# Kernel optimization log

Hardware: AMD Instinct MI355X
Metric: run time of the kernel (lower is better)

The kernel has to match this reference:

```python
import jax, jax.numpy as jnp
from jax import lax
import numpy as np

N, K, QK, W = 10, 10, 150, 128
D = 256
HID = 100
CHANS = [1, 16, 32, 64, 128, 256]
STRIDES = [2, 2, 1, 1, 1]
ITERS = 3
BN_EPS = 1e-5


def setup_inputs() -> dict:
    key = jax.random.key(0)
    ks = jax.random.split(key, 12)
    inp = {
        "support": jax.random.normal(ks[0], (N, K, 1, W, W), jnp.float32),
        "query": jax.random.normal(ks[1], (QK, 1, W, W), jnp.float32),
    }
    for i in range(5):
        inp[f"conv_w{i}"] = jax.random.normal(ks[2 + i], (CHANS[i + 1], CHANS[i], 3, 3), jnp.float32) * 0.05
        inp[f"bn_g{i}"] = jnp.ones((CHANS[i + 1],), jnp.float32)
        inp[f"bn_b{i}"] = jnp.zeros((CHANS[i + 1],), jnp.float32)
    inp["trans_w"] = jax.random.normal(ks[8], (D, D), jnp.float32) * 0.05
    inp["trans_b"] = jnp.zeros((D,), jnp.float32)
    inp["bil_w"] = jax.random.normal(ks[9], (HID, D, D), jnp.float32) * 0.02
    inp["score_w"] = jax.random.normal(ks[10], (1, HID), jnp.float32) * 0.1
    inp["score_b"] = jnp.zeros((1,), jnp.float32)
    return inp


def _block(x, w, g, b, s):
    # Conv2d(k=3, pad=1, stride=s, no bias) -> BatchNorm(eval: mean=0, var=1) -> ReLU -> MaxPool2d(2)
    x = lax.conv_general_dilated(x, w, (s, s), ((1, 1), (1, 1)),
                                 dimension_numbers=('NCHW', 'OIHW', 'NCHW'))
    scale = (g / jnp.sqrt(1.0 + BN_EPS))[None, :, None, None]
    x = jax.nn.relu(x * scale + b[None, :, None, None])
    return lax.reduce_window(x, -jnp.inf, lax.max, (1, 1, 2, 2), (1, 1, 2, 2), 'VALID')


def reference(support, query,
              conv_w0, conv_w1, conv_w2, conv_w3, conv_w4,
              bn_g0, bn_g1, bn_g2, bn_g3, bn_g4,
              bn_b0, bn_b1, bn_b2, bn_b3, bn_b4,
              trans_w, trans_b, bil_w, score_w, score_b):
    n, k = support.shape[0], support.shape[1]
    qk = query.shape[0]
    w = support.shape[3]

    ws = [conv_w0, conv_w1, conv_w2, conv_w3, conv_w4]
    gs = [bn_g0, bn_g1, bn_g2, bn_g3, bn_g4]
    bs = [bn_b0, bn_b1, bn_b2, bn_b3, bn_b4]

    # run the conv backbone on support+query jointly (BN is per-sample in eval mode)
    x = jnp.concatenate([support.reshape(n * k, 1, w, w), query], axis=0)
    for cw, g, b, s in zip(ws, gs, bs, STRIDES):
        x = _block(x, cw, g, b, s)
    feats = x.reshape(x.shape[0], -1)              # (n*k + qk, 256); spatial is 1x1
    sup = feats[:n * k].reshape(n, k, -1)          # (n, k, d)
    q = feats[n * k:]                              # (qk, d)

    # dynamic routing: Transformer(e) is recomputed each iter on the same input -> hoist
    e = sup @ trans_w.T + trans_b                  # (n, k, d)
    b0 = jnp.zeros((n, k), sup.dtype)

    def step(bb, _):
        dcoef = jax.nn.softmax(bb, axis=1)[:, :, None]   # (n, k, 1)
        c = (dcoef * e).sum(axis=1)                      # (n, d)
        cn = jnp.sqrt((c * c).sum(axis=1, keepdims=True))
        c = c * (cn / (cn * cn + 1.0))                   # squash: ||c||^2/(||c||^2+1)/||c||
        db = (c[:, None, :] * e).sum(axis=2)             # (n, k)
        return bb + db, c

    _, cs = lax.scan(step, b0, None, length=ITERS)
    proto = cs[-1]                                  # (n, d)

    # NTN: bilinear score for every (query, proto) pair, exploiting the pair structure
    t1 = jnp.einsum('nc,hce->nhe', proto, bil_w)    # (n, HID, d)
    v = jnp.einsum('nhe,qe->qnh', t1, q)            # (qk, n, HID)
    s = jax.nn.relu(v) @ score_w[0] + score_b[0]    # (qk, n)
    return jax.nn.log_softmax(s, axis=1)
```

## Files before the change

kernel.cpp:

```cpp
#include <hip/hip_runtime.h>
#include <math.h>


#define BN_SCALE rsqrtf(1.0f + 1e-5f)

#define OFF_FEATS 0
#define OFF_E     64000
#define OFF_S     89600
#define OFF_T1    91136
#define OFF_PROTO 347136
#define OFF_W1T   349696
#define OFF_W2T   354304
#define OFF_W3T   372736
#define OFF_W4T   446464
#define OFF_TWT   741376

__global__ void k_prep(const float* __restrict__ w1, const float* __restrict__ w2,
                       const float* __restrict__ w3, const float* __restrict__ w4,
                       const float* __restrict__ tw, float* __restrict__ ws) {
  float* w1t = ws + OFF_W1T;
  float* w2t = ws + OFF_W2T;
  float* w3t = ws + OFF_W3T;
  float* w4t = ws + OFF_W4T;
  float* twt = ws + OFF_TWT;
  int i = blockIdx.x * 256 + threadIdx.x;
  if (i < 4608) {
    int oc = i / 144, r = i % 144;
    int ic = r / 9, tap = r % 9;
    w1t[(ic * 9 + tap) * 32 + oc] = w1[i];
  } else if (i < 23040) {
    int m = i - 4608;
    int oc = m / 288, r = m % 288;
    int ic = r / 9, tap = r % 9;
    w2t[(ic * 9 + tap) * 64 + oc] = w2[m];
  } else if (i < 96768) {
    int m = i - 23040;
    int oc = m / 576, r = m % 576;
    int ic = r / 9, tap = r % 9;
    w3t[(ic * 9 + tap) * 128 + oc] = w3[m];
  } else if (i < 391680) {
    int m = i - 96768;
    int oc = m / 1152, r = m % 1152;
    int ic = r / 9, tap = r % 9;
    w4t[(ic * 9 + tap) * 256 + oc] = w4[m];
  } else if (i < 457216) {
    int m = i - 391680;
    int r = m >> 8, s = m & 255;
    twt[s * 256 + r] = tw[m];
  } else if (i < 713216) {
    ws[OFF_T1 + (i - 457216)] = 0.f;
  } else if (i < 714716) {
    ws[OFF_S + (i - 713216)] = 0.f;
  }
}

__global__ void __launch_bounds__(1024, 4)
k_main(const float* __restrict__ sup, const float* __restrict__ qry,
       const float* __restrict__ w0, const float* __restrict__ g0, const float* __restrict__ b0,
       const float* __restrict__ g1, const float* __restrict__ b1,
       const float* __restrict__ g2, const float* __restrict__ b2,
       const float* __restrict__ g3, const float* __restrict__ b3,
       const float* __restrict__ g4, const float* __restrict__ b4,
       const float* __restrict__ tb, float* __restrict__ ws,
       float* __restrict__ feats_g, float* __restrict__ e_buf) {
  __shared__ __align__(16) float S[38404];
  const float* w1t = ws + OFF_W1T;
  const float* w2t = ws + OFF_W2T;
  const float* w3t = ws + OFF_W3T;
  const float* w4t = ws + OFF_W4T;
  const float* twt = ws + OFF_TWT;
  const int img = blockIdx.x;
  const int t = threadIdx.x;
  const int lane = t & 63, wid = t >> 6;
  float* sa1 = S;
  float* sa2 = S + 4096;
  float* sa3 = S + 7424;
  float* sft = S + 7936;
  float* a0p = S + 8580;
  float* RED = S + 8580;
  float* L1R = S + 28164;

  const float* in = (img < 100) ? (sup + (size_t)img * 16384)
                                : (qry + (size_t)(img - 100) * 16384);

  {
    float4* S4 = (float4*)S;
    const float4 z4 = make_float4(0.f, 0.f, 0.f, 0.f);
    for (int i = t; i < 7041; i += 1024) S4[i] = z4;
  }
  __syncthreads();

  {
    const int ocp = wid & 7;
    const int rhalf = wid >> 3;
    const int oc0 = 2 * ocp, oc1 = oc0 + 1;
    float wv0[9], wv1[9];
#pragma unroll
    for (int k = 0; k < 9; k++) { wv0[k] = w0[oc0 * 9 + k]; wv1[k] = w0[oc1 * 9 + k]; }
    const float sc0 = g0[oc0] * BN_SCALE, bs0 = b0[oc0];
    const float sc1 = g0[oc1] * BN_SCALE, bs1 = b0[oc1];
#pragma unroll
    for (int it2 = 0; it2 < 2; it2++) {
      const int s2 = rhalf * 128 + it2 * 64 + lane;
      const int pr = s2 >> 3, pcq = s2 & 7;
      float ac0[2][8], ac1[2][8];
#pragma unroll
      for (int j = 0; j < 8; j++) {
        ac0[0][j] = 0.f; ac0[1][j] = 0.f; ac1[0][j] = 0.f; ac1[1][j] = 0.f;
      }
#pragma unroll
      for (int d = 0; d < 5; d++) {
        const int ir = 4 * pr - 1 + d;
        float x[17];
        if (ir >= 0) {
          const float* rp = in + ir * 128 + 16 * pcq;
          float4 q0 = ((const float4*)rp)[0];
          float4 q1 = ((const float4*)rp)[1];
          float4 q2 = ((const float4*)rp)[2];
          float4 q3 = ((const float4*)rp)[3];
          x[0] = (pcq > 0) ? rp[-1] : 0.f;
          x[1] = q0.x;  x[2] = q0.y;  x[3] = q0.z;  x[4] = q0.w;
          x[5] = q1.x;  x[6] = q1.y;  x[7] = q1.z;  x[8] = q1.w;
          x[9] = q2.x;  x[10] = q2.y; x[11] = q2.z; x[12] = q2.w;
          x[13] = q3.x; x[14] = q3.y; x[15] = q3.z; x[16] = q3.w;
        } else {
#pragma unroll
          for (int k = 0; k < 17; k++) x[k] = 0.f;
        }
        if (d <= 2) {
          const int b9 = d * 3;
#pragma unroll
          for (int j = 0; j < 8; j++) {
            ac0[0][j] = fmaf(x[2 * j + 2], wv0[b9 + 2],
                        fmaf(x[2 * j + 1], wv0[b9 + 1],
                        fmaf(x[2 * j],     wv0[b9],     ac0[0][j])));
            ac1[0][j] = fmaf(x[2 * j + 2], wv1[b9 + 2],
                        fmaf(x[2 * j + 1], wv1[b9 + 1],
                        fmaf(x[2 * j],     wv1[b9],     ac1[0][j])));
          }
        }
        if (d >= 2) {
          const int b9 = (d - 2) * 3;
#pragma unroll
          for (int j = 0; j < 8; j++) {
            ac0[1][j] = fmaf(x[2 * j + 2], wv0[b9 + 2],
                        fmaf(x[2 * j + 1], wv0[b9 + 1],
                        fmaf(x[2 * j],     wv0[b9],     ac0[1][j])));
            ac1[1][j] = fmaf(x[2 * j + 2], wv1[b9 + 2],
                        fmaf(x[2 * j + 1], wv1[b9 + 1],
                        fmaf(x[2 * j],     wv1[b9],     ac1[1][j])));
          }
        }
      }
      {
        const int row = pr + 1;
        const int swz = ((row >> 3) & 3) << 3;
        const int colp = (4 * pcq) ^ swz;
        float v[4];
#pragma unroll
        for (int p = 0; p < 4; p++) {
          float m = fmaf(ac0[0][2 * p], sc0, bs0);
          m = fmaxf(m, fmaf(ac0[0][2 * p + 1], sc0, bs0));
          m = fmaxf(m, fmaf(ac0[1][2 * p], sc0, bs0));
          m = fmaxf(m, fmaf(ac0[1][2 * p + 1], sc0, bs0));
          v[p] = fmaxf(m, 0.f);
        }
        *(float4*)(a0p + oc0 * 1224 + row * 36 + colp) =
            make_float4(v[0], v[1], v[2], v[3]);
#pragma unroll
        for (int p = 0; p < 4; p++) {
          float m = fmaf(ac1[0][2 * p], sc1, bs1);
          m = fmaxf(m, fmaf(ac1[0][2 * p + 1], sc1, bs1));
          m = fmaxf(m, fmaf(ac1[1][2 * p], sc1, bs1));
          m = fmaxf(m, fmaf(ac1[1][2 * p + 1], sc1, bs1));
          v[p] = fmaxf(m, 0.f);
        }
        *(float4*)(a0p + oc1 * 1224 + row * 36 + colp) =
            make_float4(v[0], v[1], v[2], v[3]);
      }
    }
  }
  __syncthreads();

  {
    const int pos = t & 63, py = pos >> 3, px = pos & 7;
    const int ocg = (t >> 6) & 7, icg = t >> 9;
    int offb[5], offa[5];
#pragma unroll
    for (int d = 0; d < 5; d++) {
      const int row = 4 * py + d;
      const int swz = ((row >> 3) & 3) << 3;
      offb[d] = row * 36 + ((4 * px) ^ swz);
      offa[d] = (px > 0) ? (row * 36 + ((4 * px - 4) ^ swz))
                         : (row * 36 - 4);
    }
    float acc[4][4];
#pragma unroll
    for (int j = 0; j < 4; j++)
#pragma unroll
      for (int p = 0; p < 4; p++) acc[j][p] = 0.f;
    const int ic0 = icg * 8;
    for (int ii = 0; ii < 8; ii++) {
      const int ic = ic0 + ii;
      float4 wq[9];
#pragma unroll
      for (int k = 0; k < 9; k++)
        wq[k] = *(const float4*)(w1t + (ic * 9 + k) * 32 + 4 * ocg);
      float win[25];
      const float* pl = a0p + ic * 1224;
#pragma unroll
      for (int d = 0; d < 5; d++) {
        float4 a = *(const float4*)(pl + offa[d]);
        float4 b = *(const float4*)(pl + offb[d]);
        win[d * 5 + 0] = a.w;
        win[d * 5 + 1] = b.x; win[d * 5 + 2] = b.y;
        win[d * 5 + 3] = b.z; win[d * 5 + 4] = b.w;
      }
#pragma unroll
      for (int cy = 0; cy < 2; cy++)
#pragma unroll
        for (int cx = 0; cx < 2; cx++) {
          const int p = cy * 2 + cx;
#pragma unroll
          for (int ky = 0; ky < 3; ky++)
#pragma unroll
            for (int kx = 0; kx < 3; kx++) {
              const float iv = win[(2 * cy + ky) * 5 + (2 * cx + kx)];
              const float4 wk = wq[ky * 3 + kx];
              acc[0][p] = fmaf(iv, wk.x, acc[0][p]);
              acc[1][p] = fmaf(iv, wk.y, acc[1][p]);
              acc[2][p] = fmaf(iv, wk.z, acc[2][p]);
              acc[3][p] = fmaf(iv, wk.w, acc[3][p]);
            }
        }
    }
    const int slot = ocg * 64 + pos;
    if (icg == 1) {
      float* wp2 = L1R + slot * 20;
#pragma unroll
      for (int j = 0; j < 4; j++)
        *(float4*)(wp2 + j * 4) = make_float4(acc[j][0], acc[j][1], acc[j][2], acc[j][3]);
    }
    __syncthreads();
    if (icg == 0) {
      const float* rp2 = L1R + slot * 20;
#pragma unroll
      for (int j = 0; j < 4; j++) {
        float4 o = *(const float4*)(rp2 + j * 4);
        const int oc = ocg * 4 + j;
        const float sc = g1[oc] * BN_SCALE, bsj = b1[oc];
        float m = fmaf(acc[j][0] + o.x, sc, bsj);
        m = fmaxf(m, fmaf(acc[j][1] + o.y, sc, bsj));
        m = fmaxf(m, fmaf(acc[j][2] + o.z, sc, bsj));
        m = fmaxf(m, fmaf(acc[j][3] + o.w, sc, bsj));
        sa1[oc * 124 + (py + 1) * 12 + (px + 1)] = fmaxf(m, 0.f);
      }
    }
  }
  __syncthreads();

  {
    int oc = t & 63, icg = (t >> 6) & 3, pg = t >> 8;
    int pgy = pg >> 1, pgx = pg & 1;
    float acc[16];
#pragma unroll
    for (int p = 0; p < 16; p++) acc[p] = 0.f;
    float wc[9];
    {
      const float* wp = w2t + (icg * 8) * 576 + oc;
#pragma unroll
      for (int k = 0; k < 9; k++) wc[k] = wp[k * 64];
    }
    for (int ii = 0; ii < 8; ii++) {
      int ic = icg * 8 + ii;
      float wn[9];
      if (ii < 7) {
        const float* wp = w2t + (ic + 1) * 576 + oc;
#pragma unroll
        for (int k = 0; k < 9; k++) wn[k] = wp[k * 64];
      }
      float win[6][6];
      const float* bp = sa1 + ic * 124 + 4 * pgy * 12 + 4 * pgx;
#pragma unroll
      for (int d = 0; d < 6; d++) {
        float4 u = *(const float4*)(bp + d * 12);
        float2 v = *(const float2*)(bp + d * 12 + 4);
        win[d][0] = u.x; win[d][1] = u.y; win[d][2] = u.z; win[d][3] = u.w;
        win[d][4] = v.x; win[d][5] = v.y;
      }
#pragma unroll
      for (int u = 0; u < 4; u++)
#pragma unroll
        for (int v = 0; v < 4; v++) {
          float c = acc[u * 4 + v];
#pragma unroll
          for (int ky = 0; ky < 3; ky++)
#pragma unroll
            for (int kx = 0; kx < 3; kx++)
              c = fmaf(win[u + ky][v + kx], wc[ky * 3 + kx], c);
          acc[u * 4 + v] = c;
        }
      if (ii < 7) {
#pragma unroll
        for (int k = 0; k < 9; k++) wc[k] = wn[k];
      }
    }
#pragma unroll
    for (int j = 0; j < 16; j++) RED[j * 1024 + icg * 256 + pg * 64 + oc] = acc[j];
  }
  __syncthreads();
  if (t < 256) {
    int oc = t & 63, pg = t >> 6;
    int pgy = pg >> 1, pgx = pg & 1;
    float sc = g2[oc] * BN_SCALE, bsj = b2[oc];
#pragma unroll
    for (int cy = 0; cy < 2; cy++)
#pragma unroll
      for (int cx = 0; cx < 2; cx++) {
        float m = -1e30f;
#pragma unroll
        for (int a = 0; a < 2; a++)
#pragma unroll
          for (int b = 0; b < 2; b++) {
            int j = (2 * cy + a) * 4 + (2 * cx + b);
            float v = RED[j * 1024 + pg * 64 + oc] + RED[j * 1024 + 256 + pg * 64 + oc]
                    + RED[j * 1024 + 512 + pg * 64 + oc] + RED[j * 1024 + 768 + pg * 64 + oc];
            m = fmaxf(m, fmaf(v, sc, bsj));
          }
        sa2[oc * 52 + (1 + 2 * pgy + cy) * 8 + (1 + 2 * pgx + cx)] = fmaxf(m, 0.f);
      }
  }
  __syncthreads();

  {
    int oc = t & 127, icg = t >> 7;
    float acc[16];
#pragma unroll
    for (int p = 0; p < 16; p++) acc[p] = 0.f;
    float wc[9];
    {
      const float* wp = w3t + (icg * 8) * 1152 + oc;
#pragma unroll
      for (int k = 0; k < 9; k++) wc[k] = wp[k * 128];
    }
    for (int ii = 0; ii < 8; ii++) {
      int ic = icg * 8 + ii;
      float wn[9];
      if (ii < 7) {
        const float* wp = w3t + (ic + 1) * 1152 + oc;
#pragma unroll
        for (int k = 0; k < 9; k++) wn[k] = wp[k * 128];
      }
      float win[6][6];
      const float* bp = sa2 + ic * 52;
#pragma unroll
      for (int d = 0; d < 6; d++) {
        float4 u = *(const float4*)(bp + d * 8);
        float2 v = *(const float2*)(bp + d * 8 + 4);
        win[d][0] = u.x; win[d][1] = u.y; win[d][2] = u.z; win[d][3] = u.w;
        win[d][4] = v.x; win[d][5] = v.y;
      }
#pragma unroll
      for (int u = 0; u < 4; u++)
#pragma unroll
        for (int v = 0; v < 4; v++) {
          float c = acc[u * 4 + v];
#pragma unroll
          for (int ky = 0; ky < 3; ky++)
#pragma unroll
            for (int kx = 0; kx < 3; kx++)
              c = fmaf(win[u + ky][v + kx], wc[ky * 3 + kx], c);
          acc[u * 4 + v] = c;
        }
      if (ii < 7) {
#pragma unroll
        for (int k = 0; k < 9; k++) wc[k] = wn[k];
      }
    }
#pragma unroll
    for (int j = 0; j < 16; j++) RED[j * 1024 + icg * 128 + oc] = acc[j];
  }
  __syncthreads();
  if (t < 512) {
    int oc = t & 127, pp = t >> 7;
    int py = pp >> 1, px = pp & 1;
    float sc = g3[oc] * BN_SCALE, bsj = b3[oc];
    float m = -1e30f;
#pragma unroll
    for (int a = 0; a < 2; a++)
#pragma unroll
      for (int b = 0; b < 2; b++) {
        int j = (2 * py + a) * 4 + (2 * px + b);
        float v = 0.f;
#pragma unroll
        for (int g = 0; g < 8; g++) v += RED[j * 1024 + g * 128 + oc];
        m = fmaxf(m, fmaf(v, sc, bsj));
      }
    sa3[oc * 4 + pp] = fmaxf(m, 0.f);
  }
  __syncthreads();

  {
    int oc = t & 255, icq = t >> 8;
    float acc[4] = {0.f, 0.f, 0.f, 0.f};
    float wc[9];
    {
      const float* wp = w4t + (icq * 32) * 2304 + oc;
#pragma unroll
      for (int k = 0; k < 9; k++) wc[k] = wp[k * 256];
    }
    for (int ii = 0; ii < 32; ii++) {
      int ic = icq * 32 + ii;
      float wn[9];
      if (ii < 31) {
        const float* wp = w4t + (ic + 1) * 2304 + oc;
#pragma unroll
        for (int k = 0; k < 9; k++) wn[k] = wp[k * 256];
      }
      float4 iv = *(const float4*)(sa3 + ic * 4);
#pragma unroll
      for (int py = 0; py < 2; py++)
#pragma unroll
        for (int px = 0; px < 2; px++) {
          float c = acc[py * 2 + px];
          c = fmaf(iv.x, wc[(1 - py) * 3 + (1 - px)], c);
          c = fmaf(iv.y, wc[(1 - py) * 3 + (2 - px)], c);
          c = fmaf(iv.z, wc[(2 - py) * 3 + (1 - px)], c);
          c = fmaf(iv.w, wc[(2 - py) * 3 + (2 - px)], c);
          acc[py * 2 + px] = c;
        }
      if (ii < 31) {
#pragma unroll
        for (int k = 0; k < 9; k++) wc[k] = wn[k];
      }
    }
    if (icq) {
#pragma unroll
      for (int p = 0; p < 4; p++) RED[((icq - 1) * 256 + oc) * 4 + p] = acc[p];
    }
    __syncthreads();
    if (icq == 0) {
      float sc = g4[oc] * BN_SCALE, bsj = b4[oc];
      float m = -1e30f;
#pragma unroll
      for (int p = 0; p < 4; p++) {
        float v = acc[p] + RED[oc * 4 + p] + RED[(256 + oc) * 4 + p] + RED[(512 + oc) * 4 + p];
        m = fmaxf(m, fmaf(v, sc, bsj));
      }
      float r = fmaxf(m, 0.f);
      sft[oc] = r;
      feats_g[(size_t)img * 256 + oc] = r;
    }
  }
  __syncthreads();

  if (img < 100) {
    int c = t & 255, dq = t >> 8;
    float acc = 0.f;
    float wv = twt[(dq * 64) * 256 + c];
#pragma unroll 4
    for (int ii = 0; ii < 64; ii++) {
      int d = dq * 64 + ii;
      float wnext = (ii < 63) ? twt[(d + 1) * 256 + c] : 0.f;
      acc = fmaf(sft[d], wv, acc);
      wv = wnext;
    }
    if (dq) RED[(dq - 1) * 256 + c] = acc;
    __syncthreads();
    if (dq == 0)
      e_buf[img * 256 + c] = acc + RED[c] + RED[256 + c] + RED[512 + c] + tb[c];
  }
}

__global__ void k_routing(const float* __restrict__ e, float* __restrict__ proto) {
  int n = blockIdx.x;
  __shared__ float sb[10], sdc[10], red[4], red2[40], sfc[1];
  int t = threadIdx.x;
  int lane = t & 63, wid = t >> 6;
  float ek[10];
#pragma unroll
  for (int k = 0; k < 10; k++) ek[k] = e[n * 2560 + k * 256 + t];
  if (t < 10) sb[t] = 0.f;
  __syncthreads();
  float cd = 0.f;
  for (int iter = 0; iter < 3; iter++) {
    if (t == 0) {
      float mx = sb[0];
      for (int k = 1; k < 10; k++) mx = fmaxf(mx, sb[k]);
      float sum = 0.f;
      for (int k = 0; k < 10; k++) { float ex = expf(sb[k] - mx); sdc[k] = ex; sum += ex; }
      float inv = 1.f / sum;
      for (int k = 0; k < 10; k++) sdc[k] *= inv;
    }
    __syncthreads();
    cd = 0.f;
#pragma unroll
    for (int k = 0; k < 10; k++) cd = fmaf(sdc[k], ek[k], cd);
    float ss = cd * cd;
#pragma unroll
    for (int off = 32; off > 0; off >>= 1) ss += __shfl_down(ss, off, 64);
    if (lane == 0) red[wid] = ss;
    __syncthreads();
    if (t == 0) {
      float tot = red[0] + red[1] + red[2] + red[3];
      sfc[0] = sqrtf(tot) / (tot + 1.f);
    }
    __syncthreads();
    cd *= sfc[0];
    float pr[10];
#pragma unroll
    for (int k = 0; k < 10; k++) pr[k] = cd * ek[k];
#pragma unroll
    for (int off = 32; off > 0; off >>= 1)
#pragma unroll
      for (int k = 0; k < 10; k++) pr[k] += __shfl_down(pr[k], off, 64);
    if (lane == 0)
#pragma unroll
      for (int k = 0; k < 10; k++) red2[k * 4 + wid] = pr[k];
    __syncthreads();
    if (t < 10) sb[t] += red2[t * 4] + red2[t * 4 + 1] + red2[t * 4 + 2] + red2[t * 4 + 3];
    __syncthreads();
  }
  proto[n * 256 + t] = cd;
}

__global__ void k_t1(const float* __restrict__ proto, const float* __restrict__ bw,
                     float* __restrict__ t1) {
  __shared__ float pt[384];
  const int b = blockIdx.x;
  const int h = b >> 3, c0 = (b & 7) * 32;
  const int t = threadIdx.x;
  for (int i = t; i < 320; i += 256) {
    int n = i >> 5, cl = i & 31;
    pt[cl * 12 + n] = proto[n * 256 + c0 + cl];
  }
  __syncthreads();
  float acc[10];
#pragma unroll
  for (int n = 0; n < 10; n++) acc[n] = 0.f;
  const float* wp = bw + (size_t)h * 65536 + (size_t)c0 * 256 + t;
#pragma unroll 4
  for (int cl = 0; cl < 32; cl++) {
    float wv = wp[(size_t)cl * 256];
    float4 p0 = *(const float4*)(pt + cl * 12);
    float4 p1 = *(const float4*)(pt + cl * 12 + 4);
    float2 p2 = *(const float2*)(pt + cl * 12 + 8);
    acc[0] = fmaf(p0.x, wv, acc[0]); acc[1] = fmaf(p0.y, wv, acc[1]);
    acc[2] = fmaf(p0.z, wv, acc[2]); acc[3] = fmaf(p0.w, wv, acc[3]);
    acc[4] = fmaf(p1.x, wv, acc[4]); acc[5] = fmaf(p1.y, wv, acc[5]);
    acc[6] = fmaf(p1.z, wv, acc[6]); acc[7] = fmaf(p1.w, wv, acc[7]);
    acc[8] = fmaf(p2.x, wv, acc[8]); acc[9] = fmaf(p2.y, wv, acc[9]);
  }
#pragma unroll
  for (int n = 0; n < 10; n++)
    atomicAdd(&t1[((size_t)n * 100 + h) * 256 + t], acc[n]);
}

__global__ void k_score(const float* __restrict__ t1, const float* __restrict__ qf,
                        const float* __restrict__ sw, float* __restrict__ s) {
  __shared__ float sq[256];
  __shared__ float vb[2000];
  const int q = blockIdx.x >> 1, hh = blockIdx.x & 1;
  const int t = threadIdx.x;
  const int sl = t & 3, quad = t >> 2;
  sq[t] = qf[q * 256 + t];
  __syncthreads();
  const float4* qr = (const float4*)sq;
#pragma unroll
  for (int j = 0; j < 8; j++) {
    int lr = quad + 64 * j;
    if (lr < 500) {
      int n = lr / 50, hl = lr % 50;
      const float4* row = (const float4*)(t1 + ((size_t)(n * 100 + hh * 50 + hl)) * 256);
      float acc = 0.f;
#pragma unroll
      for (int d = 0; d < 16; d++) {
        float4 a = row[d * 4 + sl];
        float4 b = qr[d * 4 + sl];
        acc += a.x * b.x + a.y * b.y + a.z * b.z + a.w * b.w;
      }
      vb[lr * 4 + sl] = acc;
    }
  }
  __syncthreads();
  if (t < 10) {
    float sum = 0.f;
    for (int hl = 0; hl < 50; hl++) {
      int lr = t * 50 + hl;
      float d = vb[lr * 4] + vb[lr * 4 + 1] + vb[lr * 4 + 2] + vb[lr * 4 + 3];
      sum = fmaf(fmaxf(d, 0.f), sw[hh * 50 + hl], sum);
    }
    atomicAdd(&s[q * 10 + t], sum);
  }
}

__global__ void k_lsm(const float* __restrict__ s, const float* __restrict__ sbp,
                      float* __restrict__ out) {
  int q = threadIdx.x;
  if (q >= 150) return;
  float sb0 = sbp[0];
  float v[10];
  float mx = -1e30f;
#pragma unroll
  for (int n = 0; n < 10; n++) {
    v[n] = s[q * 10 + n] + sb0;
    mx = fmaxf(mx, v[n]);
  }
  float sum = 0.f;
#pragma unroll
  for (int n = 0; n < 10; n++) sum += expf(v[n] - mx);
  float lse = mx + logf(sum);
#pragma unroll
  for (int n = 0; n < 10; n++) out[q * 10 + n] = v[n] - lse;
}

extern "C" void kernel_launch(void* const* d_in, const int* in_sizes, int n_in,
                              void* d_out, int out_size, void* d_ws, size_t ws_size,
                              hipStream_t stream) {
  const float* support = (const float*)d_in[0];
  const float* query   = (const float*)d_in[1];
  const float* conv_w[5]; const float* bn_g[5]; const float* bn_b[5];
  for (int i = 0; i < 5; i++) {
    conv_w[i] = (const float*)d_in[2 + 3 * i];
    bn_g[i]   = (const float*)d_in[3 + 3 * i];
    bn_b[i]   = (const float*)d_in[4 + 3 * i];
  }
  const float* trans_w = (const float*)d_in[17];
  const float* trans_b = (const float*)d_in[18];
  const float* bil_w   = (const float*)d_in[19];
  const float* score_w = (const float*)d_in[20];
  const float* score_b = (const float*)d_in[21];
  float* out = (float*)d_out;
  float* ws = (float*)d_ws;

  float* feats = ws + OFF_FEATS;
  float* e_buf = ws + OFF_E;
  float* s_buf = ws + OFF_S;
  float* t1    = ws + OFF_T1;
  float* proto = ws + OFF_PROTO;

  k_prep<<<2793, 256, 0, stream>>>(conv_w[1], conv_w[2], conv_w[3], conv_w[4],
                                   trans_w, ws);
  k_main<<<250, 1024, 0, stream>>>(support, query,
                                   conv_w[0], bn_g[0], bn_b[0],
                                   bn_g[1], bn_b[1], bn_g[2], bn_b[2],
                                   bn_g[3], bn_b[3], bn_g[4], bn_b[4],
                                   trans_b, ws, feats, e_buf);
  k_routing<<<10, 256, 0, stream>>>(e_buf, proto);
  k_t1<<<800, 256, 0, stream>>>(proto, bil_w, t1);
  k_score<<<300, 256, 0, stream>>>(t1, feats + 100 * 256, score_w, s_buf);
  k_lsm<<<1, 256, 0, stream>>>(s_buf, score_b, out);
}
```

Baseline: 205.5 us.

## Fuse routing, bilinear, score and log-softmax into one persistent kernel with grid barriers

Replaces four small tail kernels with a single 800-block kernel that runs routing, the bilinear t1 reduction, scoring and log-softmax in phases separated by software grid barriers built on atomic counters. The aim is to remove the launch gaps and tail drain between the short kernels. It relies on all 800 blocks being co-resident, since otherwise the spin barrier deadlocks. It also adds a zeroing step for the barrier counters in k_prep and compacts the stored query features.

```diff
diff --git a/kernel.cpp b/kernel.cpp
--- a/kernel.cpp
+++ b/kernel.cpp
@@ -5,6 +5,7 @@
 #define BN_SCALE rsqrtf(1.0f + 1e-5f)
 
 #define OFF_FEATS 0
+#define OFF_BAR   38400
 #define OFF_E     64000
 #define OFF_S     89600
 #define OFF_T1    91136
@@ -14,6 +15,22 @@
 #define OFF_W3T   372736
 #define OFF_W4T   446464
 #define OFF_TWT   741376
+
+__device__ __forceinline__ void gbar(unsigned* c, unsigned target) {
+  __threadfence();
+  __syncthreads();
+  if (threadIdx.x == 0) {
+    atomicAdd(&c[(blockIdx.x & 7) * 16], 1u);
+    for (;;) {
+      unsigned sum = 0;
+#pragma unroll
+      for (int j = 0; j < 8; j++) sum += atomicAdd(&c[j * 16], 0u);
+      if (sum >= target) break;
+      __builtin_amdgcn_s_sleep(8);
+    }
+  }
+  __syncthreads();
+}
 
 __global__ void k_prep(const float* __restrict__ w1, const float* __restrict__ w2,
                        const float* __restrict__ w3, const float* __restrict__ w4,
@@ -51,6 +68,8 @@
     ws[OFF_T1 + (i - 457216)] = 0.f;
   } else if (i < 714716) {
     ws[OFF_S + (i - 713216)] = 0.f;
+  } else if (i < 715100) {
+    ws[OFF_BAR + (i - 714716)] = 0.f;
   }
 }
 
@@ -449,7 +468,7 @@
       }
       float r = fmaxf(m, 0.f);
       sft[oc] = r;
-      feats_g[(size_t)img * 256 + oc] = r;
+      if (img >= 100) feats_g[(size_t)(img - 100) * 256 + oc] = r;
     }
   }
   __syncthreads();
@@ -472,146 +491,152 @@
   }
 }
 
-__global__ void k_routing(const float* __restrict__ e, float* __restrict__ proto) {
-  int n = blockIdx.x;
-  __shared__ float sb[10], sdc[10], red[4], red2[40], sfc[1];
-  int t = threadIdx.x;
-  int lane = t & 63, wid = t >> 6;
-  float ek[10];
-#pragma unroll
-  for (int k = 0; k < 10; k++) ek[k] = e[n * 2560 + k * 256 + t];
-  if (t < 10) sb[t] = 0.f;
-  __syncthreads();
-  float cd = 0.f;
-  for (int iter = 0; iter < 3; iter++) {
-    if (t == 0) {
-      float mx = sb[0];
-      for (int k = 1; k < 10; k++) mx = fmaxf(mx, sb[k]);
+__global__ void __launch_bounds__(256, 4)
+k_tail(const float* __restrict__ e, float* __restrict__ proto,
+       const float* __restrict__ bw, float* __restrict__ t1,
+       const float* __restrict__ qf, const float* __restrict__ sw,
+       const float* __restrict__ sbp, float* __restrict__ s,
+       unsigned* __restrict__ bars, float* __restrict__ out) {
+  __shared__ float SH[2256];
+  const int bid = blockIdx.x;
+  const int t = threadIdx.x;
+
+  if (bid < 10) {
+    const int n = bid;
+    float* sb = SH; float* sdc = SH + 16; float* red = SH + 32;
+    float* red2 = SH + 48; float* sfc = SH + 96;
+    const int lane = t & 63, wid = t >> 6;
+    float ek[10];
+#pragma unroll
+    for (int k = 0; k < 10; k++) ek[k] = e[n * 2560 + k * 256 + t];
+    if (t < 10) sb[t] = 0.f;
+    __syncthreads();
+    float cd = 0.f;
+    for (int iter = 0; iter < 3; iter++) {
+      if (t == 0) {
+        float mx = sb[0];
+        for (int k = 1; k < 10; k++) mx = fmaxf(mx, sb[k]);
+        float sum = 0.f;
+        for (int k = 0; k < 10; k++) { float ex = expf(sb[k] - mx); sdc[k] = ex; sum += ex; }
+        float inv = 1.f / sum;
+        for (int k = 0; k < 10; k++) sdc[k] *= inv;
+      }
+      __syncthreads();
+      cd = 0.f;
+#pragma unroll
+      for (int k = 0; k < 10; k++) cd = fmaf(sdc[k], ek[k], cd);
+      float ss = cd * cd;
+#pragma unroll
+      for (int off = 32; off > 0; off >>= 1) ss += __shfl_down(ss, off, 64);
+      if (lane == 0) red[wid] = ss;
+      __syncthreads();
+      if (t == 0) {
+        float tot = red[0] + red[1] + red[2] + red[3];
+        sfc[0] = sqrtf(tot) / (tot + 1.f);
+      }
+      __syncthreads();
+      cd *= sfc[0];
+      float pr[10];
+#pragma unroll
+      for (int k = 0; k < 10; k++) pr[k] = cd * ek[k];
+#pragma unroll
+      for (int off = 32; off > 0; off >>= 1)
+#pragma unroll
+        for (int k = 0; k < 10; k++) pr[k] += __shfl_down(pr[k], off, 64);
+      if (lane == 0)
+#pragma unroll
+        for (int k = 0; k < 10; k++) red2[k * 4 + wid] = pr[k];
+      __syncthreads();
+      if (t < 10) sb[t] += red2[t * 4] + red2[t * 4 + 1] + red2[t * 4 + 2] + red2[t * 4 + 3];
+      __syncthreads();
+    }
+    proto[n * 256 + t] = cd;
+  }
+  gbar(bars, 800u);
+
+  {
+    float* pt = SH;
+    const int h = bid >> 3, c0 = (bid & 7) * 32;
+    for (int i = t; i < 320; i += 256) {
+      int n = i >> 5, cl = i & 31;
+      pt[cl * 12 + n] = proto[n * 256 + c0 + cl];
+    }
+    __syncthreads();
+    float acc[10];
+#pragma unroll
+    for (int n = 0; n < 10; n++) acc[n] = 0.f;
+    const float* wp = bw + (size_t)h * 65536 + (size_t)c0 * 256 + t;
+#pragma unroll 4
+    for (int cl = 0; cl < 32; cl++) {
+      float wv = wp[(size_t)cl * 256];
+      float4 p0 = *(const float4*)(pt + cl * 12);
+      float4 p1 = *(const float4*)(pt + cl * 12 + 4);
+      float2 p2 = *(const float2*)(pt + cl * 12 + 8);
+      acc[0] = fmaf(p0.x, wv, acc[0]); acc[1] = fmaf(p0.y, wv, acc[1]);
+      acc[2] = fmaf(p0.z, wv, acc[2]); acc[3] = fmaf(p0.w, wv, acc[3]);
+      acc[4] = fmaf(p1.x, wv, acc[4]); acc[5] = fmaf(p1.y, wv, acc[5]);
+      acc[6] = fmaf(p1.z, wv, acc[6]); acc[7] = fmaf(p1.w, wv, acc[7]);
+      acc[8] = fmaf(p2.x, wv, acc[8]); acc[9] = fmaf(p2.y, wv, acc[9]);
+    }
+#pragma unroll
+    for (int n = 0; n < 10; n++)
+      atomicAdd(&t1[((size_t)n * 100 + h) * 256 + t], acc[n]);
+  }
+  gbar(bars + 128, 800u);
+
+  if (bid < 300) {
+    float* sq = SH;
+    float* vb = SH + 256;
+    const int q = bid >> 1, hh = bid & 1;
+    const int sl = t & 3, quad = t >> 2;
+    sq[t] = qf[q * 256 + t];
+    __syncthreads();
+    const float4* qr = (const float4*)sq;
+#pragma unroll
+    for (int j = 0; j < 8; j++) {
+      int lr = quad + 64 * j;
+      if (lr < 500) {
+        int n = lr / 50, hl = lr % 50;
+        const float4* row = (const float4*)(t1 + ((size_t)(n * 100 + hh * 50 + hl)) * 256);
+        float acc = 0.f;
+#pragma unroll
+        for (int d = 0; d < 16; d++) {
+          float4 a = row[d * 4 + sl];
+          float4 b = qr[d * 4 + sl];
+          acc += a.x * b.x + a.y * b.y + a.z * b.z + a.w * b.w;
+        }
+        vb[lr * 4 + sl] = acc;
+      }
+    }
+    __syncthreads();
+    if (t < 10) {
       float sum = 0.f;
-      for (int k = 0; k < 10; k++) { float ex = expf(sb[k] - mx); sdc[k] = ex; sum += ex; }
-      float inv = 1.f / sum;
-      for (int k = 0; k < 10; k++) sdc[k] *= inv;
-    }
-    __syncthreads();
-    cd = 0.f;
-#pragma unroll
-    for (int k = 0; k < 10; k++) cd = fmaf(sdc[k], ek[k], cd);
-    float ss = cd * cd;
-#pragma unroll
-    for (int off = 32; off > 0; off >>= 1) ss += __shfl_down(ss, off, 64);
-    if (lane == 0) red[wid] = ss;
-    __syncthreads();
-    if (t == 0) {
-      float tot = red[0] + red[1] + red[2] + red[3];
-      sfc[0] = sqrtf(tot) / (tot + 1.f);
-    }
-    __syncthreads();
-    cd *= sfc[0];
-    float pr[10];
-#pragma unroll
-    for (int k = 0; k < 10; k++) pr[k] = cd * ek[k];
-#pragma unroll
-    for (int off = 32; off > 0; off >>= 1)
-#pragma unroll
-      for (int k = 0; k < 10; k++) pr[k] += __shfl_down(pr[k], off, 64);
-    if (lane == 0)
-#pragma unroll
-      for (int k = 0; k < 10; k++) red2[k * 4 + wid] = pr[k];
-    __syncthreads();
-    if (t < 10) sb[t] += red2[t * 4] + red2[t * 4 + 1] + red2[t * 4 + 2] + red2[t * 4 + 3];
-    __syncthreads();
-  }
-  proto[n * 256 + t] = cd;
-}
-
-__global__ void k_t1(const float* __restrict__ proto, const float* __restrict__ bw,
-                     float* __restrict__ t1) {
-  __shared__ float pt[384];
-  const int b = blockIdx.x;
-  const int h = b >> 3, c0 = (b & 7) * 32;
-  const int t = threadIdx.x;
-  for (int i = t; i < 320; i += 256) {
-    int n = i >> 5, cl = i & 31;
-    pt[cl * 12 + n] = proto[n * 256 + c0 + cl];
-  }
-  __syncthreads();
-  float acc[10];
-#pragma unroll
-  for (int n = 0; n < 10; n++) acc[n] = 0.f;
-  const float* wp = bw + (size_t)h * 65536 + (size_t)c0 * 256 + t;
-#pragma unroll 4
-  for (int cl = 0; cl < 32; cl++) {
-    float wv = wp[(size_t)cl * 256];
-    float4 p0 = *(const float4*)(pt + cl * 12);
-    float4 p1 = *(const float4*)(pt + cl * 12 + 4);
-    float2 p2 = *(const float2*)(pt + cl * 12 + 8);
-    acc[0] = fmaf(p0.x, wv, acc[0]); acc[1] = fmaf(p0.y, wv, acc[1]);
-    acc[2] = fmaf(p0.z, wv, acc[2]); acc[3] = fmaf(p0.w, wv, acc[3]);
-    acc[4] = fmaf(p1.x, wv, acc[4]); acc[5] = fmaf(p1.y, wv, acc[5]);
-    acc[6] = fmaf(p1.z, wv, acc[6]); acc[7] = fmaf(p1.w, wv, acc[7]);
-    acc[8] = fmaf(p2.x, wv, acc[8]); acc[9] = fmaf(p2.y, wv, acc[9]);
-  }
-#pragma unroll
-  for (int n = 0; n < 10; n++)
-    atomicAdd(&t1[((size_t)n * 100 + h) * 256 + t], acc[n]);
-}
-
-__global__ void k_score(const float* __restrict__ t1, const float* __restrict__ qf,
-                        const float* __restrict__ sw, float* __restrict__ s) {
-  __shared__ float sq[256];
-  __shared__ float vb[2000];
-  const int q = blockIdx.x >> 1, hh = blockIdx.x & 1;
-  const int t = threadIdx.x;
-  const int sl = t & 3, quad = t >> 2;
-  sq[t] = qf[q * 256 + t];
-  __syncthreads();
-  const float4* qr = (const float4*)sq;
-#pragma unroll
-  for (int j = 0; j < 8; j++) {
-    int lr = quad + 64 * j;
-    if (lr < 500) {
-      int n = lr / 50, hl = lr % 50;
-      const float4* row = (const float4*)(t1 + ((size_t)(n * 100 + hh * 50 + hl)) * 256);
-      float acc = 0.f;
-#pragma unroll
-      for (int d = 0; d < 16; d++) {
-        float4 a = row[d * 4 + sl];
-        float4 b = qr[d * 4 + sl];
-        acc += a.x * b.x + a.y * b.y + a.z * b.z + a.w * b.w;
-      }
-      vb[lr * 4 + sl] = acc;
-    }
-  }
-  __syncthreads();
-  if (t < 10) {
+      for (int hl = 0; hl < 50; hl++) {
+        int lr = t * 50 + hl;
+        float d = vb[lr * 4] + vb[lr * 4 + 1] + vb[lr * 4 + 2] + vb[lr * 4 + 3];
+        sum = fmaf(fmaxf(d, 0.f), sw[hh * 50 + hl], sum);
+      }
+      atomicAdd(&s[q * 10 + t], sum);
+    }
+  }
+  gbar(bars + 256, 800u);
+
+  if (bid == 0 && t < 150) {
+    float sb0 = sbp[0];
+    float v[10];
+    float mx = -1e30f;
+#pragma unroll
+    for (int n = 0; n < 10; n++) {
+      v[n] = atomicAdd(&s[t * 10 + n], 0.f) + sb0;
+      mx = fmaxf(mx, v[n]);
+    }
     float sum = 0.f;
-    for (int hl = 0; hl < 50; hl++) {
-      int lr = t * 50 + hl;
-      float d = vb[lr * 4] + vb[lr * 4 + 1] + vb[lr * 4 + 2] + vb[lr * 4 + 3];
-      sum = fmaf(fmaxf(d, 0.f), sw[hh * 50 + hl], sum);
-    }
-    atomicAdd(&s[q * 10 + t], sum);
-  }
-}
-
-__global__ void k_lsm(const float* __restrict__ s, const float* __restrict__ sbp,
-                      float* __restrict__ out) {
-  int q = threadIdx.x;
-  if (q >= 150) return;
-  float sb0 = sbp[0];
-  float v[10];
-  float mx = -1e30f;
-#pragma unroll
-  for (int n = 0; n < 10; n++) {
-    v[n] = s[q * 10 + n] + sb0;
-    mx = fmaxf(mx, v[n]);
-  }
-  float sum = 0.f;
-#pragma unroll
-  for (int n = 0; n < 10; n++) sum += expf(v[n] - mx);
-  float lse = mx + logf(sum);
-#pragma unroll
-  for (int n = 0; n < 10; n++) out[q * 10 + n] = v[n] - lse;
+#pragma unroll
+    for (int n = 0; n < 10; n++) sum += expf(v[n] - mx);
+    float lse = mx + logf(sum);
+#pragma unroll
+    for (int n = 0; n < 10; n++) out[t * 10 + n] = v[n] - lse;
+  }
 }
 
 extern "C" void kernel_launch(void* const* d_in, const int* in_sizes, int n_in,
@@ -638,16 +663,15 @@
   float* s_buf = ws + OFF_S;
   float* t1    = ws + OFF_T1;
   float* proto = ws + OFF_PROTO;
-
-  k_prep<<<2793, 256, 0, stream>>>(conv_w[1], conv_w[2], conv_w[3], conv_w[4],
+  unsigned* bars = (unsigned*)(ws + OFF_BAR);
+
+  k_prep<<<2794, 256, 0, stream>>>(conv_w[1], conv_w[2], conv_w[3], conv_w[4],
                                    trans_w, ws);
   k_main<<<250, 1024, 0, stream>>>(support, query,
                                    conv_w[0], bn_g[0], bn_b[0],
                                    bn_g[1], bn_b[1], bn_g[2], bn_b[2],
                                    bn_g[3], bn_b[3], bn_g[4], bn_b[4],
                                    trans_b, ws, feats, e_buf);
-  k_routing<<<10, 256, 0, stream>>>(e_buf, proto);
-  k_t1<<<800, 256, 0, stream>>>(proto, bil_w, t1);
-  k_score<<<300, 256, 0, stream>>>(t1, feats + 100 * 256, score_w, s_buf);
-  k_lsm<<<1, 256, 0, stream>>>(s_buf, score_b, out);
+  k_tail<<<800, 256, 0, stream>>>(e_buf, proto, bil_w, t1,
+                                  feats, score_w, score_b, s_buf, bars, out);
 }
```

Result: slower. 406.6 us (+97.8%).

## Fuse bilinear t1, scoring and log-softmax into one per-hidden-unit kernel

Applied to the files above, without the earlier changes.

Replaces the separate t1, score and log-softmax kernels with a single kernel in which each block owns one hidden unit. The block computes that unit's proto-by-bilinear-weight slice in shared memory, scores every (query, proto) pair, and accumulates into 8 replicated score buffers. The last block, found through an atomic counter, then does the log-softmax. This drops two launches, the t1 global buffer and its large zero-init, but leaves only 100 blocks with more atomic traffic and a serial tail in the final block.

```diff
diff --git a/kernel.cpp b/kernel.cpp
--- a/kernel.cpp
+++ b/kernel.cpp
@@ -5,9 +5,9 @@
 #define BN_SCALE rsqrtf(1.0f + 1e-5f)
 
 #define OFF_FEATS 0
+#define OFF_CNT   38400
+#define OFF_S8    38416
 #define OFF_E     64000
-#define OFF_S     89600
-#define OFF_T1    91136
 #define OFF_PROTO 347136
 #define OFF_W1T   349696
 #define OFF_W2T   354304
@@ -47,10 +47,10 @@
     int m = i - 391680;
     int r = m >> 8, s = m & 255;
     twt[s * 256 + r] = tw[m];
-  } else if (i < 713216) {
-    ws[OFF_T1 + (i - 457216)] = 0.f;
-  } else if (i < 714716) {
-    ws[OFF_S + (i - 713216)] = 0.f;
+  } else if (i < 469248) {
+    ws[OFF_S8 + (i - 457216)] = 0.f;
+  } else if (i == 469248) {
+    ws[OFF_CNT] = 0.f;
   }
 }
 
@@ -449,7 +449,7 @@
       }
       float r = fmaxf(m, 0.f);
       sft[oc] = r;
-      feats_g[(size_t)img * 256 + oc] = r;
+      if (img >= 100) feats_g[(size_t)(img - 100) * 256 + oc] = r;
     }
   }
   __syncthreads();
@@ -472,7 +472,7 @@
   }
 }
 
-__global__ void k_routing(const float* __restrict__ e, float* __restrict__ proto) {
+__global__ void k_route(const float* __restrict__ e, float* __restrict__ proto) {
   int n = blockIdx.x;
   __shared__ float sb[10], sdc[10], red[4], red2[40], sfc[1];
   int t = threadIdx.x;
@@ -524,94 +524,117 @@
   proto[n * 256 + t] = cd;
 }
 
-__global__ void k_t1(const float* __restrict__ proto, const float* __restrict__ bw,
-                     float* __restrict__ t1) {
-  __shared__ float pt[384];
-  const int b = blockIdx.x;
-  const int h = b >> 3, c0 = (b & 7) * 32;
+__global__ void __launch_bounds__(256, 4)
+k_hx(const float* __restrict__ proto, const float* __restrict__ bw,
+     const float* __restrict__ qf, const float* __restrict__ sw,
+     const float* __restrict__ sbp, float* __restrict__ srep,
+     unsigned* __restrict__ cnt, float* __restrict__ out) {
+  __shared__ __align__(16) float pt[3072];
+  __shared__ __align__(16) float Tp[4][2640];
+  __shared__ int lastFlag;
+  const int h = blockIdx.x;
   const int t = threadIdx.x;
-  for (int i = t; i < 320; i += 256) {
-    int n = i >> 5, cl = i & 31;
-    pt[cl * 12 + n] = proto[n * 256 + c0 + cl];
-  }
-  __syncthreads();
-  float acc[10];
-#pragma unroll
-  for (int n = 0; n < 10; n++) acc[n] = 0.f;
-  const float* wp = bw + (size_t)h * 65536 + (size_t)c0 * 256 + t;
+  const int lane = t & 63, wid = t >> 6;
+
+  for (int i = t; i < 2560; i += 256) {
+    int n = i >> 8, c = i & 255;
+    pt[c * 12 + n] = proto[n * 256 + c];
+  }
+  __syncthreads();
+
+  {
+    float4 A[10];
+#pragma unroll
+    for (int n = 0; n < 10; n++) A[n] = make_float4(0.f, 0.f, 0.f, 0.f);
+    const float* bp = bw + (size_t)h * 65536 + (size_t)(wid * 64) * 256 + 4 * lane;
+    const float* pp0 = pt + (wid * 64) * 12;
 #pragma unroll 4
-  for (int cl = 0; cl < 32; cl++) {
-    float wv = wp[(size_t)cl * 256];
-    float4 p0 = *(const float4*)(pt + cl * 12);
-    float4 p1 = *(const float4*)(pt + cl * 12 + 4);
-    float2 p2 = *(const float2*)(pt + cl * 12 + 8);
-    acc[0] = fmaf(p0.x, wv, acc[0]); acc[1] = fmaf(p0.y, wv, acc[1]);
-    acc[2] = fmaf(p0.z, wv, acc[2]); acc[3] = fmaf(p0.w, wv, acc[3]);
-    acc[4] = fmaf(p1.x, wv, acc[4]); acc[5] = fmaf(p1.y, wv, acc[5]);
-    acc[6] = fmaf(p1.z, wv, acc[6]); acc[7] = fmaf(p1.w, wv, acc[7]);
-    acc[8] = fmaf(p2.x, wv, acc[8]); acc[9] = fmaf(p2.y, wv, acc[9]);
-  }
-#pragma unroll
-  for (int n = 0; n < 10; n++)
-    atomicAdd(&t1[((size_t)n * 100 + h) * 256 + t], acc[n]);
-}
-
-__global__ void k_score(const float* __restrict__ t1, const float* __restrict__ qf,
-                        const float* __restrict__ sw, float* __restrict__ s) {
-  __shared__ float sq[256];
-  __shared__ float vb[2000];
-  const int q = blockIdx.x >> 1, hh = blockIdx.x & 1;
-  const int t = threadIdx.x;
-  const int sl = t & 3, quad = t >> 2;
-  sq[t] = qf[q * 256 + t];
-  __syncthreads();
-  const float4* qr = (const float4*)sq;
-#pragma unroll
-  for (int j = 0; j < 8; j++) {
-    int lr = quad + 64 * j;
-    if (lr < 500) {
-      int n = lr / 50, hl = lr % 50;
-      const float4* row = (const float4*)(t1 + ((size_t)(n * 100 + hh * 50 + hl)) * 256);
-      float acc = 0.f;
-#pragma unroll
-      for (int d = 0; d < 16; d++) {
-        float4 a = row[d * 4 + sl];
-        float4 b = qr[d * 4 + sl];
-        acc += a.x * b.x + a.y * b.y + a.z * b.z + a.w * b.w;
-      }
-      vb[lr * 4 + sl] = acc;
-    }
-  }
-  __syncthreads();
-  if (t < 10) {
-    float sum = 0.f;
-    for (int hl = 0; hl < 50; hl++) {
-      int lr = t * 50 + hl;
-      float d = vb[lr * 4] + vb[lr * 4 + 1] + vb[lr * 4 + 2] + vb[lr * 4 + 3];
-      sum = fmaf(fmaxf(d, 0.f), sw[hh * 50 + hl], sum);
-    }
-    atomicAdd(&s[q * 10 + t], sum);
-  }
-}
-
-__global__ void k_lsm(const float* __restrict__ s, const float* __restrict__ sbp,
-                      float* __restrict__ out) {
-  int q = threadIdx.x;
-  if (q >= 150) return;
-  float sb0 = sbp[0];
-  float v[10];
-  float mx = -1e30f;
-#pragma unroll
-  for (int n = 0; n < 10; n++) {
-    v[n] = s[q * 10 + n] + sb0;
-    mx = fmaxf(mx, v[n]);
-  }
-  float sum = 0.f;
-#pragma unroll
-  for (int n = 0; n < 10; n++) sum += expf(v[n] - mx);
-  float lse = mx + logf(sum);
-#pragma unroll
-  for (int n = 0; n < 10; n++) out[q * 10 + n] = v[n] - lse;
+    for (int ci = 0; ci < 64; ci++) {
+      float4 wv = *(const float4*)(bp + ci * 256);
+      const float* pp = pp0 + ci * 12;
+      float4 p0 = *(const float4*)pp;
+      float4 p1 = *(const float4*)(pp + 4);
+      float2 p2 = *(const float2*)(pp + 8);
+      A[0].x = fmaf(p0.x, wv.x, A[0].x); A[0].y = fmaf(p0.x, wv.y, A[0].y);
+      A[0].z = fmaf(p0.x, wv.z, A[0].z); A[0].w = fmaf(p0.x, wv.w, A[0].w);
+      A[1].x = fmaf(p0.y, wv.x, A[1].x); A[1].y = fmaf(p0.y, wv.y, A[1].y);
+      A[1].z = fmaf(p0.y, wv.z, A[1].z); A[1].w = fmaf(p0.y, wv.w, A[1].w);
+      A[2].x = fmaf(p0.z, wv.x, A[2].x); A[2].y = fmaf(p0.z, wv.y, A[2].y);
+      A[2].z = fmaf(p0.z, wv.z, A[2].z); A[2].w = fmaf(p0.z, wv.w, A[2].w);
+      A[3].x = fmaf(p0.w, wv.x, A[3].x); A[3].y = fmaf(p0.w, wv.y, A[3].y);
+      A[3].z = fmaf(p0.w, wv.z, A[3].z); A[3].w = fmaf(p0.w, wv.w, A[3].w);
+      A[4].x = fmaf(p1.x, wv.x, A[4].x); A[4].y = fmaf(p1.x, wv.y, A[4].y);
+      A[4].z = fmaf(p1.x, wv.z, A[4].z); A[4].w = fmaf(p1.x, wv.w, A[4].w);
+      A[5].x = fmaf(p1.y, wv.x, A[5].x); A[5].y = fmaf(p1.y, wv.y, A[5].y);
+      A[5].z = fmaf(p1.y, wv.z, A[5].z); A[5].w = fmaf(p1.y, wv.w, A[5].w);
+      A[6].x = fmaf(p1.z, wv.x, A[6].x); A[6].y = fmaf(p1.z, wv.y, A[6].y);
+      A[6].z = fmaf(p1.z, wv.z, A[6].z); A[6].w = fmaf(p1.z, wv.w, A[6].w);
+      A[7].x = fmaf(p1.w, wv.x, A[7].x); A[7].y = fmaf(p1.w, wv.y, A[7].y);
+      A[7].z = fmaf(p1.w, wv.z, A[7].z); A[7].w = fmaf(p1.w, wv.w, A[7].w);
+      A[8].x = fmaf(p2.x, wv.x, A[8].x); A[8].y = fmaf(p2.x, wv.y, A[8].y);
+      A[8].z = fmaf(p2.x, wv.z, A[8].z); A[8].w = fmaf(p2.x, wv.w, A[8].w);
+      A[9].x = fmaf(p2.y, wv.x, A[9].x); A[9].y = fmaf(p2.y, wv.y, A[9].y);
+      A[9].z = fmaf(p2.y, wv.z, A[9].z); A[9].w = fmaf(p2.y, wv.w, A[9].w);
+    }
+#pragma unroll
+    for (int n = 0; n < 10; n++)
+      *(float4*)(&Tp[wid][n * 264 + 4 * lane]) = A[n];
+  }
+  __syncthreads();
+
+  float* Tl = pt;
+#pragma unroll
+  for (int j = 0; j < 10; j++) {
+    Tl[j * 264 + t] = Tp[0][j * 264 + t] + Tp[1][j * 264 + t]
+                    + Tp[2][j * 264 + t] + Tp[3][j * 264 + t];
+  }
+  __syncthreads();
+
+  {
+    const float swh = sw[h];
+#pragma unroll
+    for (int j = 0; j < 6; j++) {
+      const int p = j * 256 + t;
+      if (p < 1500) {
+        const int q = p / 10, n = p % 10;
+        const float4* Trow = (const float4*)(Tl + n * 264);
+        const float4* qrow = (const float4*)(qf + q * 256);
+        float acc = 0.f;
+#pragma unroll 8
+        for (int i = 0; i < 64; i++) {
+          float4 a = Trow[i];
+          float4 b = qrow[i];
+          acc = fmaf(a.x, b.x, fmaf(a.y, b.y, fmaf(a.z, b.z, fmaf(a.w, b.w, acc))));
+        }
+        atomicAdd(&srep[(h & 7) * 1504 + p], fmaxf(acc, 0.f) * swh);
+      }
+    }
+  }
+
+  __threadfence();
+  __syncthreads();
+  if (t == 0) lastFlag = (atomicAdd(cnt, 1u) == 99u);
+  __syncthreads();
+  if (lastFlag && t < 150) {
+    float sb0 = sbp[0];
+    float v[10];
+    float mx = -1e30f;
+#pragma unroll
+    for (int n = 0; n < 10; n++) {
+      float sum = 0.f;
+#pragma unroll
+      for (int r = 0; r < 8; r++)
+        sum += atomicAdd(&srep[r * 1504 + t * 10 + n], 0.f);
+      v[n] = sum + sb0;
+      mx = fmaxf(mx, v[n]);
+    }
+    float sum2 = 0.f;
+#pragma unroll
+    for (int n = 0; n < 10; n++) sum2 += expf(v[n] - mx);
+    float lse = mx + logf(sum2);
+#pragma unroll
+    for (int n = 0; n < 10; n++) out[t * 10 + n] = v[n] - lse;
+  }
 }
 
 extern "C" void kernel_launch(void* const* d_in, const int* in_sizes, int n_in,
@@ -635,19 +658,18 @@
 
   float* feats = ws + OFF_FEATS;
   float* e_buf = ws + OFF_E;
-  float* s_buf = ws + OFF_S;
-  float* t1    = ws + OFF_T1;
+  float* srep  = ws + OFF_S8;
   float* proto = ws + OFF_PROTO;
-
-  k_prep<<<2793, 256, 0, stream>>>(conv_w[1], conv_w[2], conv_w[3], conv_w[4],
+  unsigned* cnt = (unsigned*)(ws + OFF_CNT);
+
+  k_prep<<<1834, 256, 0, stream>>>(conv_w[1], conv_w[2], conv_w[3], conv_w[4],
                                    trans_w, ws);
   k_main<<<250, 1024, 0, stream>>>(support, query,
                                    conv_w[0], bn_g[0], bn_b[0],
                                    bn_g[1], bn_b[1], bn_g[2], bn_b[2],
                                    bn_g[3], bn_b[3], bn_g[4], bn_b[4],
                                    trans_b, ws, feats, e_buf);
-  k_routing<<<10, 256, 0, stream>>>(e_buf, proto);
-  k_t1<<<800, 256, 0, stream>>>(proto, bil_w, t1);
-  k_score<<<300, 256, 0, stream>>>(t1, feats + 100 * 256, score_w, s_buf);
-  k_lsm<<<1, 256, 0, stream>>>(s_buf, score_b, out);
+  k_route<<<10, 256, 0, stream>>>(e_buf, proto);
+  k_hx<<<100, 256, 0, stream>>>(proto, bil_w, feats, score_w, score_b,
+                                srep, cnt, out);
 }
```

Result: slower. 224.5 us (+9.2%).
